# Kernel tuning notes

Measured on AMD Instinct MI355X. Metric: run time of the kernel, lower is better.

The kernel has to match this reference:

```python
import jax, jax.numpy as jnp
import numpy as np

B, IN, ED, PW, OUT, CL, NK = 2048, 4096, 8192, 2048, 256, 16, 32
MIX = 0.5

def _onehot_mask(key, n):
    # near-one-hot selector matrix [n, NK], as built by forward_update_masks
    idx = jax.random.choice(key, n, (NK,), replace=False)
    return jnp.zeros((n, NK), jnp.float32).at[idx, jnp.arange(NK)].set(1.0)

def setup_inputs():
    ks = jax.random.split(jax.random.key(0), 24)
    f = jnp.float32
    adj = (jax.random.uniform(ks[4], (IN, IN)) < 0.01).astype(f)
    adj = jnp.maximum(adj, adj.T).at[jnp.arange(IN), jnp.arange(IN)].set(1.0)
    return {
        'x_gene': jax.random.normal(ks[0], (B, IN), f),
        'x_invmea': jax.random.normal(ks[1], (B, IN), f),
        'x_curv': jax.random.normal(ks[2], (B, ED), f),
        'clinn': jax.random.normal(ks[3], (B, CL), f),
        'Adj': adj,
        'edge_mask': (jax.random.uniform(ks[5], (ED, IN)) < 0.005).astype(f),
        'pathway_mask': (jax.random.uniform(ks[6], (PW, ED)) < 0.02).astype(f),
        'top_gene_mask': _onehot_mask(ks[7], IN),
        'top_invmea_mask': _onehot_mask(ks[8], IN),
        'top_curv_mask': _onehot_mask(ks[9], ED),
        'top_path_mask': _onehot_mask(ks[10], PW),
        'W1': jnp.full((IN, IN), 0.05, f),
        'b1': 0.01 * jax.random.normal(ks[11], (IN,), f),
        'W2': jnp.full((ED, IN), 0.05, f),
        'b2': 0.01 * jax.random.normal(ks[12], (ED,), f),
        'W3': jnp.full((PW, ED), 0.05, f),
        'b3': 0.01 * jax.random.normal(ks[13], (PW,), f),
        'W4': 0.02 * jax.random.normal(ks[14], (OUT, PW), f),
        'b4': 0.01 * jax.random.normal(ks[15], (OUT,), f),
        'W5': 0.02 * jax.random.normal(ks[16], (OUT, OUT), f),
        'b5': 0.01 * jax.random.normal(ks[17], (OUT,), f),
        'W6': 0.05 * jax.random.normal(ks[18], (OUT, OUT + CL + 4 * NK), f),
        'W7': 0.05 * jax.random.normal(ks[19], (1, OUT), f),
        'mp11': MIX * jnp.ones(IN, f),
        'mp12': (1.0 - MIX) * jnp.ones(IN, f),
        'mp1': jnp.ones(IN, f),
        'mp21': MIX * jnp.ones(ED, f),
        'mp22': (1.0 - MIX) * jnp.ones(ED, f),
        'mp2': jnp.ones(ED, f),
        'mp3': jnp.ones(PW, f),
    }

def reference(x_gene, x_invmea, x_curv, clinn, Adj, edge_mask, pathway_mask,
              top_gene_mask, top_invmea_mask, top_curv_mask, top_path_mask,
              W1, b1, W2, b2, W3, b3, W4, b4, W5, b5, W6, W7,
              mp11, mp12, mp1, mp21, mp22, mp2, mp3):
    sg = jax.lax.stop_gradient
    sig = jax.nn.sigmoid
    kept_gene = sg(x_gene @ top_gene_mask)                     # [B,NK] gather-as-matmul
    x1 = sig(x_gene @ (W1 * Adj).T + b1)                       # masked linear [B,IN]
    x1 = x_invmea * (mp11 * mp1) + x1 * (mp12 * mp1)
    kept_invmea = sg(x1 @ top_invmea_mask)
    x1 = sig(x1 @ (W2 * edge_mask).T + b2)                     # [B,ED]
    x1 = x_curv * (mp21 * mp2) + x1 * (mp22 * mp2)
    kept_curv = sg(x1 @ top_curv_mask)
    x1 = sig(x1 @ (W3 * pathway_mask).T + b3)                  # [B,PW]
    x1 = x1 * mp3
    kept_path = sg(x1 @ top_path_mask)
    x1 = sig(x1 @ W4.T + b4)
    x1 = sig(x1 @ W5.T + b5)                                   # [B,OUT]
    x_cat = jnp.concatenate([x1, kept_gene, kept_invmea, kept_curv, kept_path, clinn], axis=1)
    lp = sig(x_cat @ W6.T)
    lp = lp - jnp.mean(lp, axis=1, keepdims=True)
    return lp @ W7.T                                           # [B,1]
```

## Files before the change

kernel.cpp:

```cpp
#include <hip/hip_runtime.h>

typedef unsigned short u16;
typedef __attribute__((ext_vector_type(4))) float f32x4;
typedef __attribute__((ext_vector_type(8))) short s16x8;

__device__ __forceinline__ u16 f2bf(float f) {
    union { float f; unsigned u; } c; c.f = f;
    return (u16)((c.u + 0x7fffu + ((c.u >> 16) & 1u)) >> 16);
}
__device__ __forceinline__ float bf2f(u16 u) {
    union { unsigned u; float f; } c; c.u = ((unsigned)u) << 16; return c.f;
}
__device__ __forceinline__ unsigned pk2(float a, float b) {
    return (unsigned)f2bf(a) | ((unsigned)f2bf(b) << 16);
}
__device__ __forceinline__ float sigm(float x) { return 1.0f / (1.0f + __expf(-x)); }
__device__ __forceinline__ void fma2(unsigned xv, float w, float& a0, float& a1) {
    union { float f; unsigned u; } lo, hi;
    lo.u = xv << 16; hi.u = xv & 0xFFFF0000u;
    a0 += w * lo.f; a1 += w * hi.f;
}

__device__ __forceinline__ void load16_g2l(const void* g, void* l) {
    __builtin_amdgcn_global_load_lds(
        (const __attribute__((address_space(1))) unsigned int*)(unsigned long long)g,
        (__attribute__((address_space(3))) unsigned int*)(unsigned int)(unsigned long long)l,
        16, 0, 0);
}

__global__ __launch_bounds__(256) void convF(const float* __restrict__ in,
                                             u16* __restrict__ out, unsigned n8) {
    unsigned i = blockIdx.x * 256u + threadIdx.x;
    if (i >= n8) return;
    float4 a = ((const float4*)in)[2 * i];
    float4 b = ((const float4*)in)[2 * i + 1];
    uint4 o;
    o.x = pk2(a.x, a.y); o.y = pk2(a.z, a.w);
    o.z = pk2(b.x, b.y); o.w = pk2(b.z, b.w);
    ((uint4*)out)[i] = o;
}

__global__ __launch_bounds__(256) void transpF(const float* __restrict__ in,
                                               u16* __restrict__ out, int Rr, int Cc) {
    __shared__ float t[64][65];
    const int r0 = blockIdx.y * 64, c0 = blockIdx.x * 64;
    const int tid = threadIdx.x;
#pragma unroll
    for (int i = 0; i < 16; i++) {
        int idx = tid + i * 256;
        int rr = idx >> 6, cc = idx & 63;
        t[rr][cc] = in[(size_t)(r0 + rr) * Cc + c0 + cc];
    }
    __syncthreads();
#pragma unroll
    for (int i = 0; i < 16; i++) {
        int idx = tid + i * 256;
        int cc = idx >> 6, rr = idx & 63;
        out[(size_t)(c0 + cc) * Rr + r0 + rr] = f2bf(t[rr][cc]);
    }
}

__global__ __launch_bounds__(256) void transpB(const u16* __restrict__ in,
                                               u16* __restrict__ out, int Rr, int Cc) {
    __shared__ u16 t[64][66];
    const int r0 = blockIdx.y * 64, c0 = blockIdx.x * 64;
    const int tid = threadIdx.x;
#pragma unroll
    for (int i = 0; i < 16; i++) {
        int idx = tid + i * 256;
        int rr = idx >> 6, cc = idx & 63;
        t[rr][cc] = in[(size_t)(r0 + rr) * Cc + c0 + cc];
    }
    __syncthreads();
#pragma unroll
    for (int i = 0; i < 16; i++) {
        int idx = tid + i * 256;
        int cc = idx >> 6, rr = idx & 63;
        out[(size_t)(c0 + cc) * Rr + r0 + rr] = t[rr][cc];
    }
}

__global__ __launch_bounds__(256) void ell_build(const float* __restrict__ M,
                                                 const float* __restrict__ W,
                                                 unsigned* __restrict__ ell,
                                                 int* __restrict__ cnt,
                                                 int C, int PAD, int R) {
    const int lane = threadIdx.x & 63;
    const int row = blockIdx.x * 4 + (threadIdx.x >> 6);
    if (row >= R) return;
    const float* mrow = M + (size_t)row * C;
    const float* wrow = W + (size_t)row * C;
    int n = 0;
    for (int c = lane * 4; c < C; c += 256) {
        float4 m = *(const float4*)(mrow + c);
        n += (m.x != 0.f) + (m.y != 0.f) + (m.z != 0.f) + (m.w != 0.f);
    }
    int pre = n;
#pragma unroll
    for (int off = 1; off < 64; off <<= 1) {
        int t = __shfl_up(pre, off, 64);
        if (lane >= off) pre += t;
    }
    int s = pre - n;
    unsigned* erow = ell + (size_t)row * PAD;
    for (int c = lane * 4; c < C; c += 256) {
        float4 m = *(const float4*)(mrow + c);
        if (m.x != 0.f) { if (s < PAD) erow[s] = ((unsigned)f2bf(wrow[c + 0]) << 16) | (unsigned)(c + 0); s++; }
        if (m.y != 0.f) { if (s < PAD) erow[s] = ((unsigned)f2bf(wrow[c + 1]) << 16) | (unsigned)(c + 1); s++; }
        if (m.z != 0.f) { if (s < PAD) erow[s] = ((unsigned)f2bf(wrow[c + 2]) << 16) | (unsigned)(c + 2); s++; }
        if (m.w != 0.f) { if (s < PAD) erow[s] = ((unsigned)f2bf(wrow[c + 3]) << 16) | (unsigned)(c + 3); s++; }
    }
    int tot = __shfl(pre, 63, 64);
    if (lane == 0) cnt[row] = tot > PAD ? PAD : tot;
}

template <int BPL>
__global__ __launch_bounds__(256) void spmm(const unsigned* __restrict__ ell,
                                            const int* __restrict__ cnt,
                                            const u16* __restrict__ xT,
                                            u16* __restrict__ outT,
                                            const float* __restrict__ bias,
                                            const float* __restrict__ c1a,
                                            const float* __restrict__ c1b,
                                            const float* __restrict__ c2a,
                                            const float* __restrict__ c2b,
                                            const u16* __restrict__ invT,
                                            int PAD) {
    const int lane = threadIdx.x & 63;
    const int wv = __builtin_amdgcn_readfirstlane((int)(threadIdx.x >> 6));
    const int j = blockIdx.y * 4 + wv;
    const int b0 = blockIdx.x * (64 * BPL) + lane * BPL;

    const unsigned* ep = ell + (size_t)j * PAD;
    int len = cnt[j];
    if (len > PAD) len = PAD;

    float acc[BPL];
#pragma unroll
    for (int i = 0; i < BPL; i++) acc[i] = 0.f;

    const int nfull = len >> 3;
    unsigned eA[8];
    if (nfull > 0) {
#pragma unroll
        for (int t = 0; t < 8; t++) eA[t] = ep[t];
    }
    for (int g = 0; g < nfull; g++) {
        unsigned eB[8];
        const bool more = (g + 1 < nfull);
        if (more) {
#pragma unroll
            for (int t = 0; t < 8; t++) eB[t] = ep[(g + 1) * 8 + t];
        }
        if (BPL == 8) {
            uint4 xv[8];
#pragma unroll
            for (int t = 0; t < 8; t++)
                xv[t] = *(const uint4*)(xT + ((size_t)(eA[t] & 0xFFFFu) << 11) + b0);
#pragma unroll
            for (int t = 0; t < 8; t++) {
                union { float f; unsigned u; } w; w.u = (eA[t] >> 16) << 16;
                fma2(xv[t].x, w.f, acc[0], acc[1]);
                fma2(xv[t].y, w.f, acc[2], acc[3]);
                fma2(xv[t].z, w.f, acc[4], acc[5]);
                fma2(xv[t].w, w.f, acc[6], acc[7]);
            }
        } else {
            uint2 xv[8];
#pragma unroll
            for (int t = 0; t < 8; t++)
                xv[t] = *(const uint2*)(xT + ((size_t)(eA[t] & 0xFFFFu) << 11) + b0);
#pragma unroll
            for (int t = 0; t < 8; t++) {
                union { float f; unsigned u; } w; w.u = (eA[t] >> 16) << 16;
                fma2(xv[t].x, w.f, acc[0], acc[1]);
                fma2(xv[t].y, w.f, acc[2], acc[3]);
            }
        }
        if (more) {
#pragma unroll
            for (int t = 0; t < 8; t++) eA[t] = eB[t];
        }
    }
    for (int s = nfull * 8; s < len; ++s) {
        unsigned e = ep[s];
        union { float f; unsigned u; } w; w.u = (e >> 16) << 16;
        const u16* xp = xT + ((size_t)(e & 0xFFFFu) << 11) + b0;
        if (BPL == 8) {
            uint4 xv = *(const uint4*)xp;
            fma2(xv.x, w.f, acc[0], acc[1]); fma2(xv.y, w.f, acc[2], acc[3]);
            fma2(xv.z, w.f, acc[4], acc[5]); fma2(xv.w, w.f, acc[6], acc[7]);
        } else {
            uint2 xv = *(const uint2*)xp;
            fma2(xv.x, w.f, acc[0], acc[1]); fma2(xv.y, w.f, acc[2], acc[3]);
        }
    }

    const float bi = bias[j];
    float c1 = 0.f;
    if (c1a) { c1 = c1a[j]; if (c1b) c1 *= c1b[j]; }
    float c2 = 1.f;
    if (c2a) { c2 = c2a[j]; if (c2b) c2 *= c2b[j]; }

    float v[BPL];
#pragma unroll
    for (int i = 0; i < BPL; i++) v[i] = sigm(acc[i] + bi) * c2;
    if (invT) {
        const unsigned long long* ip = (const unsigned long long*)(invT + ((size_t)j << 11) + b0);
#pragma unroll
        for (int h = 0; h < BPL / 4; h++) {
            unsigned long long iv = __builtin_nontemporal_load(ip + h);
            unsigned lo = (unsigned)iv, hi = (unsigned)(iv >> 32);
            union { float f; unsigned u; } g0, g1, g2, g3;
            g0.u = lo << 16; g1.u = lo & 0xFFFF0000u;
            g2.u = hi << 16; g3.u = hi & 0xFFFF0000u;
            v[4 * h + 0] += g0.f * c1; v[4 * h + 1] += g1.f * c1;
            v[4 * h + 2] += g2.f * c1; v[4 * h + 3] += g3.f * c1;
        }
    }
    unsigned long long* op = (unsigned long long*)(outT + ((size_t)j << 11) + b0);
#pragma unroll
    for (int h = 0; h < BPL / 4; h++) {
        unsigned long long ov = (unsigned long long)pk2(v[4 * h + 0], v[4 * h + 1])
                              | ((unsigned long long)pk2(v[4 * h + 2], v[4 * h + 3]) << 32);
        __builtin_nontemporal_store(ov, op + h);
    }
}

__global__ __launch_bounds__(256) void find_all(const float* __restrict__ m0, int n0,
                                                const float* __restrict__ m1, int n1,
                                                const float* __restrict__ m2, int n2,
                                                const float* __restrict__ m3, int n3,
                                                int* __restrict__ out) {
    __shared__ int red[256];
    const int g = blockIdx.x;
    const int which = g >> 5, k = g & 31;
    const float* mask; int n;
    if (which == 0)      { mask = m0; n = n0; }
    else if (which == 1) { mask = m1; n = n1; }
    else if (which == 2) { mask = m2; n = n2; }
    else                 { mask = m3; n = n3; }
    int best = -1;
    for (int i = threadIdx.x; i < n; i += 256)
        if (mask[(size_t)i * 32 + k] != 0.0f) best = i;
    red[threadIdx.x] = best;
    __syncthreads();
    for (int off = 128; off > 0; off >>= 1) {
        if (threadIdx.x < off) {
            int o = red[threadIdx.x + off];
            if (o > red[threadIdx.x]) red[threadIdx.x] = o;
        }
        __syncthreads();
    }
    if (threadIdx.x == 0) out[which * 32 + k] = red[0] < 0 ? 0 : red[0];
}

__global__ __launch_bounds__(256) void gatherFT(const float* __restrict__ src, int ld,
                                                const int* __restrict__ idx,
                                                u16* __restrict__ dstT) {
    int i = blockIdx.x * 256 + threadIdx.x;
    int kk = i >> 11, b = i & 2047;
    dstT[i] = f2bf(src[(size_t)b * ld + idx[kk]]);
}
__global__ __launch_bounds__(256) void gatherT(const u16* __restrict__ xT,
                                               const int* __restrict__ idx,
                                               u16* __restrict__ dstT) {
    int i = blockIdx.x * 256 + threadIdx.x;
    int kk = i >> 11, b = i & 2047;
    dstT[i] = xT[(size_t)idx[kk] * 2048 + b];
}

__global__ __launch_bounds__(256) void build_xcat(float* __restrict__ xcat,
                                                  const u16* __restrict__ x5,
                                                  const u16* __restrict__ kgT,
                                                  const u16* __restrict__ kiT,
                                                  const u16* __restrict__ kcT,
                                                  const u16* __restrict__ kpT,
                                                  const float* __restrict__ clinn) {
    int i = blockIdx.x * 256 + threadIdx.x;
    if (i >= 2048 * 400) return;
    int b = i / 400, c = i - b * 400;
    float v;
    if (c < 256)      v = bf2f(x5[b * 256 + c]);
    else if (c < 288) v = bf2f(kgT[(c - 256) * 2048 + b]);
    else if (c < 320) v = bf2f(kiT[(c - 288) * 2048 + b]);
    else if (c < 352) v = bf2f(kcT[(c - 320) * 2048 + b]);
    else if (c < 384) v = bf2f(kpT[(c - 352) * 2048 + b]);
    else              v = clinn[b * 16 + (c - 384)];
    xcat[i] = v;
}

template <int WR, int WC, int MF, int NF, int KC, int WPE>
__global__ __launch_bounds__(WR * WC * 64, WPE)
void gemm_t(const u16* __restrict__ A, const u16* __restrict__ W,
            u16* __restrict__ Out, const float* __restrict__ bias, int N, int K) {
    constexpr int NTHR = WR * WC * 64;
    constexpr int BM = WR * MF * 16;
    constexpr int BN = WC * NF * 16;
    constexpr int BK = KC * 32;
    constexpr int CPR = KC * 4;
    constexpr int MSK = CPR - 1;
    constexpr int CA = BM * CPR / NTHR;
    constexpr int CB = BN * CPR / NTHR;
    constexpr int L  = CA + CB;

    __shared__ u16 At[2][BM * BK];
    __shared__ u16 Bt[2][BN * BK];

    const int tid = threadIdx.x;
    const int lane = tid & 63;
    const int wave = tid >> 6;
    const int wr = wave / WC, wc = wave % WC;
    const int tn = blockIdx.x, tm = blockIdx.y;
    const int r16 = lane & 15;
    const int q = lane >> 4;

    const u16* aSrc[CA]; int aDst[CA];
#pragma unroll
    for (int j = 0; j < CA; j++) {
        int c = tid + j * NTHR;
        int r = c / CPR, p = c - r * CPR;
        aSrc[j] = A + (size_t)(tm * BM + r) * K + (p ^ (r & MSK)) * 8;
        aDst[j] = c * 8;
    }
    const u16* bSrc[CB]; int bDst[CB];
#pragma unroll
    for (int j = 0; j < CB; j++) {
        int c = tid + j * NTHR;
        int r = c / CPR, p = c - r * CPR;
        bSrc[j] = W + (size_t)(tn * BN + r) * K + (p ^ (r & MSK)) * 8;
        bDst[j] = c * 8;
    }
    int aRd[MF][KC], bRd[NF][KC];
#pragma unroll
    for (int mi = 0; mi < MF; mi++)
#pragma unroll
        for (int kc = 0; kc < KC; kc++)
            aRd[mi][kc] = (wr * MF * 16 + mi * 16 + r16) * BK + (((kc * 4 + q) ^ (r16 & MSK)) << 3);
#pragma unroll
    for (int ni = 0; ni < NF; ni++)
#pragma unroll
        for (int kc = 0; kc < KC; kc++)
            bRd[ni][kc] = (wc * NF * 16 + ni * 16 + r16) * BK + (((kc * 4 + q) ^ (r16 & MSK)) << 3);

    const int nIter = K / BK;

#define ISSUE(slot, it_)                                              \
    do {                                                              \
        const int k0_ = (it_) * BK;                                   \
        _Pragma("unroll")                                             \
        for (int j = 0; j < CA; j++)                                  \
            load16_g2l(aSrc[j] + k0_, &At[slot][aDst[j]]);            \
        _Pragma("unroll")                                             \
        for (int j = 0; j < CB; j++)                                  \
            load16_g2l(bSrc[j] + k0_, &Bt[slot][bDst[j]]);            \
    } while (0)

    ISSUE(0, 0);
    if (nIter > 1) ISSUE(1, 1);

    f32x4 acc[MF][NF];
#pragma unroll
    for (int i = 0; i < MF; i++)
#pragma unroll
        for (int j = 0; j < NF; j++) acc[i][j] = (f32x4){0.f, 0.f, 0.f, 0.f};

    for (int it = 0; it < nIter; ++it) {
        const int s = it & 1;
        if (it + 1 < nIter) __builtin_amdgcn_s_waitcnt(0xF70 | L);
        else                __builtin_amdgcn_s_waitcnt(0xF70);
        __asm__ volatile("" ::: "memory");
        __builtin_amdgcn_s_barrier();
        __asm__ volatile("" ::: "memory");

        s16x8 af[KC][MF], bfr[KC][NF];
#pragma unroll
        for (int kc = 0; kc < KC; kc++) {
#pragma unroll
            for (int mi = 0; mi < MF; mi++) af[kc][mi] = *(const s16x8*)(&At[s][aRd[mi][kc]]);
#pragma unroll
            for (int ni = 0; ni < NF; ni++) bfr[kc][ni] = *(const s16x8*)(&Bt[s][bRd[ni][kc]]);
        }
        __asm__ volatile("" ::: "memory");
        __builtin_amdgcn_s_waitcnt(0xC07F);
        __builtin_amdgcn_s_barrier();
        __asm__ volatile("" ::: "memory");

        if (it + 2 < nIter) ISSUE(s, it + 2);

#pragma unroll
        for (int kc = 0; kc < KC; kc++)
#pragma unroll
            for (int mi = 0; mi < MF; mi++)
#pragma unroll
                for (int ni = 0; ni < NF; ni++)
                    acc[mi][ni] = __builtin_amdgcn_mfma_f32_16x16x32_bf16(af[kc][mi], bfr[kc][ni], acc[mi][ni], 0, 0, 0);
    }
#undef ISSUE

#pragma unroll
    for (int ni = 0; ni < NF; ni++) {
        const int n = tn * BN + wc * NF * 16 + ni * 16 + r16;
        const float bi = bias ? bias[n] : 0.f;
#pragma unroll
        for (int mi = 0; mi < MF; mi++) {
#pragma unroll
            for (int rg = 0; rg < 4; rg++) {
                const int m = tm * BM + wr * MF * 16 + mi * 16 + q * 4 + rg;
                Out[(size_t)m * N + n] = f2bf(sigm(acc[mi][ni][rg] + bi));
            }
        }
    }
}

__global__ __launch_bounds__(256) void tail_k(const float* __restrict__ xcat,
                                              const float* __restrict__ W6,
                                              const float* __restrict__ W7,
                                              float* __restrict__ out) {
    __shared__ float xs[8 * 400];
    __shared__ float s1[4][8], s2[4][8], s3[4];
    const int tid = threadIdx.x;
    const int b0 = blockIdx.x * 8;
    for (int i = tid; i < 8 * 400; i += 256) {
        int r = i / 400, k = i - r * 400;
        xs[i] = xcat[(size_t)(b0 + r) * 400 + k];
    }
    __syncthreads();
    const int j = tid;
    float acc[8];
#pragma unroll
    for (int r = 0; r < 8; r++) acc[r] = 0.f;
    const float4* wrow = (const float4*)(W6 + (size_t)j * 400);
    for (int c = 0; c < 100; c++) {
        float4 wv = wrow[c];
        const float* wp = (const float*)&wv;
#pragma unroll
        for (int t = 0; t < 4; t++) {
            float w = wp[t];
            int k = c * 4 + t;
#pragma unroll
            for (int r = 0; r < 8; r++) acc[r] += w * xs[r * 400 + k];
        }
    }
    const float w7j = W7[j];
    const int lane = tid & 63, wave = tid >> 6;
    float t3 = w7j;
#pragma unroll
    for (int off = 32; off > 0; off >>= 1) t3 += __shfl_down(t3, off, 64);
    if (lane == 0) s3[wave] = t3;
#pragma unroll
    for (int r = 0; r < 8; r++) {
        float lp = sigm(acc[r]);
        float t1 = lp, t2 = lp * w7j;
#pragma unroll
        for (int off = 32; off > 0; off >>= 1) {
            t1 += __shfl_down(t1, off, 64);
            t2 += __shfl_down(t2, off, 64);
        }
        if (lane == 0) { s1[wave][r] = t1; s2[wave][r] = t2; }
    }
    __syncthreads();
    if (tid < 8) {
        float S1 = s1[0][tid] + s1[1][tid] + s1[2][tid] + s1[3][tid];
        float S2 = s2[0][tid] + s2[1][tid] + s2[2][tid] + s2[3][tid];
        float SW = s3[0] + s3[1] + s3[2] + s3[3];
        out[b0 + tid] = S2 - (S1 * (1.f / 256.f)) * SW;
    }
}

extern "C" void kernel_launch(void* const* d_in, const int* in_sizes, int n_in,
                              void* d_out, int out_size, void* d_ws, size_t ws_size,
                              hipStream_t stream) {
    const float* x_gene   = (const float*)d_in[0];
    const float* x_invmea = (const float*)d_in[1];
    const float* x_curv   = (const float*)d_in[2];
    const float* clinn    = (const float*)d_in[3];
    const float* Adj      = (const float*)d_in[4];
    const float* edge_m   = (const float*)d_in[5];
    const float* path_m   = (const float*)d_in[6];
    const float* tg_mask  = (const float*)d_in[7];
    const float* ti_mask  = (const float*)d_in[8];
    const float* tc_mask  = (const float*)d_in[9];
    const float* tp_mask  = (const float*)d_in[10];
    const float* W1 = (const float*)d_in[11];  const float* b1 = (const float*)d_in[12];
    const float* W2 = (const float*)d_in[13];  const float* b2 = (const float*)d_in[14];
    const float* W3 = (const float*)d_in[15];  const float* b3 = (const float*)d_in[16];
    const float* W4 = (const float*)d_in[17];  const float* b4 = (const float*)d_in[18];
    const float* W5 = (const float*)d_in[19];  const float* b5 = (const float*)d_in[20];
    const float* W6 = (const float*)d_in[21];
    const float* W7 = (const float*)d_in[22];
    const float* mp11 = (const float*)d_in[23];
    const float* mp12 = (const float*)d_in[24];
    const float* mp1  = (const float*)d_in[25];
    const float* mp21 = (const float*)d_in[26];
    const float* mp22 = (const float*)d_in[27];
    const float* mp2  = (const float*)d_in[28];
    const float* mp3  = (const float*)d_in[29];

    char* ws = (char*)d_ws;
    const float* nulf = nullptr;
    float* out = (float*)d_out;

    u16*  xTg   = (u16*)(ws + 0);
    float* xcat = (float*)(ws + 0);
    u16*  xinvT = (u16*)(ws + 16777216);
    u16*  xcvT  = (u16*)(ws + 33554432);
    u16*  x1T   = (u16*)(ws + 67108864);
    u16*  x2T   = (u16*)(ws + 83886080);
    u16*  x3T   = (u16*)(ws + 117440512);
    u16*  x3    = (u16*)(ws + 125829120);
    unsigned* ell1 = (unsigned*)(ws + 134217728);
    unsigned* ell2 = (unsigned*)(ws + 138412032);
    unsigned* ell3 = (unsigned*)(ws + 141557760);
    int* cnt1 = (int*)(ws + 144179200);
    int* cnt2 = (int*)(ws + 144195584);
    int* cnt3 = (int*)(ws + 144228352);
    int* idxg = (int*)(ws + 144236544);
    int* idxi = idxg + 32;
    int* idxc = idxg + 64;
    int* idxp = idxg + 96;
    u16* kgT  = (u16*)(ws + 144237056);
    u16* kiT  = (u16*)(ws + 144368128);
    u16* kcT  = (u16*)(ws + 144499200);
    u16* kpT  = (u16*)(ws + 144630272);
    u16* w4b  = (u16*)(ws + 144761344);
    u16* w5b  = (u16*)(ws + 145809920);
    u16* x4   = (u16*)(ws + 145940992);
    u16* x5   = (u16*)(ws + 146989568);

    find_all<<<128, 256, 0, stream>>>(tg_mask, 4096, ti_mask, 4096,
                                      tc_mask, 8192, tp_mask, 2048, idxg);
    gatherFT<<<256, 256, 0, stream>>>(x_gene, 4096, idxg, kgT);

    transpF<<<dim3(64, 32), 256, 0, stream>>>(x_gene, xTg, 2048, 4096);
    transpF<<<dim3(64, 32), 256, 0, stream>>>(x_invmea, xinvT, 2048, 4096);
    transpF<<<dim3(128, 32), 256, 0, stream>>>(x_curv, xcvT, 2048, 8192);

    ell_build<<<1024, 256, 0, stream>>>(Adj,    W1, ell1, cnt1, 4096, 256, 4096);
    ell_build<<<2048, 256, 0, stream>>>(edge_m, W2, ell2, cnt2, 4096,  96, 8192);
    ell_build<<<512,  256, 0, stream>>>(path_m, W3, ell3, cnt3, 8192, 320, 2048);

    convF<<<256, 256, 0, stream>>>(W4, w4b, 65536u);
    convF<<<32, 256, 0, stream>>>(W5, w5b, 8192u);

    spmm<8><<<dim3(4, 1024), 256, 0, stream>>>(ell1, cnt1, xTg, x1T, b1,
                                               mp11, mp1, mp12, mp1, xinvT, 256);
    gatherT<<<256, 256, 0, stream>>>(x1T, idxi, kiT);

    spmm<8><<<dim3(4, 2048), 256, 0, stream>>>(ell2, cnt2, x1T, x2T, b2,
                                               mp21, mp2, mp22, mp2, xcvT, 96);
    gatherT<<<256, 256, 0, stream>>>(x2T, idxc, kcT);

    spmm<4><<<dim3(8, 512), 256, 0, stream>>>(ell3, cnt3, x2T, x3T, b3,
                                              nulf, nulf, mp3, nulf, (const u16*)nullptr, 320);
    gatherT<<<256, 256, 0, stream>>>(x3T, idxp, kpT);
    transpB<<<dim3(32, 32), 256, 0, stream>>>(x3T, x3, 2048, 2048);

    gemm_t<2, 2, 2, 2, 2, 4><<<dim3(4, 32), 256, 0, stream>>>(x3, w4b, x4, b4, 256, 2048);
    gemm_t<2, 2, 2, 2, 2, 4><<<dim3(4, 32), 256, 0, stream>>>(x4, w5b, x5, b5, 256, 256);

    build_xcat<<<3200, 256, 0, stream>>>(xcat, x5, kgT, kiT, kcT, kpT, clinn);
    tail_k<<<256, 256, 0, stream>>>(xcat, W6, W7, out);
}
```

Measured before the change: 950.6 us.

## Merge preprocessing kernels into one launch, fold xcat build into tail, shrink spmm BPL

Folds the three input transposes, three ELL builds, the mask index search and the two weight conversions into a single prep_all kernel that dispatches on block ID. This removes many separate launches and the gaps between them. The xcat concatenation is now read directly inside tail_k, so the intermediate fp32 buffer and its extra kernel are gone. The first two spmm launches also drop from 8 to 4 batch elements per lane with twice the grid, trading per-thread reuse for more parallelism.

```diff
diff --git a/kernel.cpp b/kernel.cpp
--- a/kernel.cpp
+++ b/kernel.cpp
@@ -28,22 +28,9 @@
         16, 0, 0);
 }
 
-__global__ __launch_bounds__(256) void convF(const float* __restrict__ in,
-                                             u16* __restrict__ out, unsigned n8) {
-    unsigned i = blockIdx.x * 256u + threadIdx.x;
-    if (i >= n8) return;
-    float4 a = ((const float4*)in)[2 * i];
-    float4 b = ((const float4*)in)[2 * i + 1];
-    uint4 o;
-    o.x = pk2(a.x, a.y); o.y = pk2(a.z, a.w);
-    o.z = pk2(b.x, b.y); o.w = pk2(b.z, b.w);
-    ((uint4*)out)[i] = o;
-}
-
-__global__ __launch_bounds__(256) void transpF(const float* __restrict__ in,
-                                               u16* __restrict__ out, int Rr, int Cc) {
-    __shared__ float t[64][65];
-    const int r0 = blockIdx.y * 64, c0 = blockIdx.x * 64;
+__device__ void d_transpF(const float* __restrict__ in, u16* __restrict__ out,
+                          int Rr, int Cc, int bx, int by, float (*t)[65]) {
+    const int r0 = by * 64, c0 = bx * 64;
     const int tid = threadIdx.x;
 #pragma unroll
     for (int i = 0; i < 16; i++) {
@@ -60,33 +47,11 @@
     }
 }
 
-__global__ __launch_bounds__(256) void transpB(const u16* __restrict__ in,
-                                               u16* __restrict__ out, int Rr, int Cc) {
-    __shared__ u16 t[64][66];
-    const int r0 = blockIdx.y * 64, c0 = blockIdx.x * 64;
-    const int tid = threadIdx.x;
-#pragma unroll
-    for (int i = 0; i < 16; i++) {
-        int idx = tid + i * 256;
-        int rr = idx >> 6, cc = idx & 63;
-        t[rr][cc] = in[(size_t)(r0 + rr) * Cc + c0 + cc];
-    }
-    __syncthreads();
-#pragma unroll
-    for (int i = 0; i < 16; i++) {
-        int idx = tid + i * 256;
-        int cc = idx >> 6, rr = idx & 63;
-        out[(size_t)(c0 + cc) * Rr + r0 + rr] = t[rr][cc];
-    }
-}
-
-__global__ __launch_bounds__(256) void ell_build(const float* __restrict__ M,
-                                                 const float* __restrict__ W,
-                                                 unsigned* __restrict__ ell,
-                                                 int* __restrict__ cnt,
-                                                 int C, int PAD, int R) {
+__device__ void d_ell(const float* __restrict__ M, const float* __restrict__ W,
+                      unsigned* __restrict__ ell, int* __restrict__ cnt,
+                      int C, int PAD, int R, int bid) {
     const int lane = threadIdx.x & 63;
-    const int row = blockIdx.x * 4 + (threadIdx.x >> 6);
+    const int row = bid * 4 + (threadIdx.x >> 6);
     if (row >= R) return;
     const float* mrow = M + (size_t)row * C;
     const float* wrow = W + (size_t)row * C;
@@ -112,6 +77,80 @@
     }
     int tot = __shfl(pre, 63, 64);
     if (lane == 0) cnt[row] = tot > PAD ? PAD : tot;
+}
+
+__device__ void d_find(const float* __restrict__ mask, int n, int* __restrict__ outp,
+                       int* red) {
+    int best = -1;
+    for (int i = threadIdx.x; i < n; i += 256)
+        if (mask[(size_t)i * 32 + (blockIdx.x & 31)] != 0.0f) best = i;
+    red[threadIdx.x] = best;
+    __syncthreads();
+    for (int off = 128; off > 0; off >>= 1) {
+        if (threadIdx.x < off) {
+            int o = red[threadIdx.x + off];
+            if (o > red[threadIdx.x]) red[threadIdx.x] = o;
+        }
+        __syncthreads();
+    }
+    if (threadIdx.x == 0) *outp = red[0] < 0 ? 0 : red[0];
+}
+
+__device__ void d_conv(const float* __restrict__ in, u16* __restrict__ out,
+                       int bid, unsigned n8) {
+    unsigned i = bid * 256u + threadIdx.x;
+    if (i >= n8) return;
+    float4 a = ((const float4*)in)[2 * i];
+    float4 b = ((const float4*)in)[2 * i + 1];
+    uint4 o;
+    o.x = pk2(a.x, a.y); o.y = pk2(a.z, a.w);
+    o.z = pk2(b.x, b.y); o.w = pk2(b.z, b.w);
+    ((uint4*)out)[i] = o;
+}
+
+__global__ __launch_bounds__(256) void prep_all(
+    const float* __restrict__ xg_f, const float* __restrict__ xinv_f,
+    const float* __restrict__ xcv_f,
+    u16* __restrict__ xTg, u16* __restrict__ xinvT, u16* __restrict__ xcvT,
+    const float* __restrict__ Adj, const float* __restrict__ W1,
+    unsigned* __restrict__ ell1, int* __restrict__ cnt1,
+    const float* __restrict__ edge, const float* __restrict__ W2,
+    unsigned* __restrict__ ell2, int* __restrict__ cnt2,
+    const float* __restrict__ path, const float* __restrict__ W3,
+    unsigned* __restrict__ ell3, int* __restrict__ cnt3,
+    const float* __restrict__ m0, const float* __restrict__ m1,
+    const float* __restrict__ m2, const float* __restrict__ m3,
+    int* __restrict__ idx,
+    const float* __restrict__ W4, u16* __restrict__ w4b,
+    const float* __restrict__ W5, u16* __restrict__ w5b) {
+    __shared__ float tile[64][65];
+    int id = blockIdx.x;
+    if (id < 2048) { d_transpF(xg_f, xTg, 2048, 4096, id & 63, id >> 6, tile); return; }
+    id -= 2048;
+    if (id < 2048) { d_transpF(xinv_f, xinvT, 2048, 4096, id & 63, id >> 6, tile); return; }
+    id -= 2048;
+    if (id < 4096) { d_transpF(xcv_f, xcvT, 2048, 8192, id & 127, id >> 7, tile); return; }
+    id -= 4096;
+    if (id < 1024) { d_ell(Adj, W1, ell1, cnt1, 4096, 256, 4096, id); return; }
+    id -= 1024;
+    if (id < 2048) { d_ell(edge, W2, ell2, cnt2, 4096, 96, 8192, id); return; }
+    id -= 2048;
+    if (id < 512) { d_ell(path, W3, ell3, cnt3, 8192, 320, 2048, id); return; }
+    id -= 512;
+    if (id < 128) {
+        const float* mk; int n;
+        int which = id >> 5;
+        if (which == 0)      { mk = m0; n = 4096; }
+        else if (which == 1) { mk = m1; n = 4096; }
+        else if (which == 2) { mk = m2; n = 8192; }
+        else                 { mk = m3; n = 2048; }
+        d_find(mk, n, idx + which * 32 + (id & 31), (int*)tile);
+        return;
+    }
+    id -= 128;
+    if (id < 256) { d_conv(W4, w4b, id, 65536u); return; }
+    id -= 256;
+    d_conv(W5, w5b, id, 8192u);
 }
 
 template <int BPL>
@@ -227,34 +266,6 @@
     }
 }
 
-__global__ __launch_bounds__(256) void find_all(const float* __restrict__ m0, int n0,
-                                                const float* __restrict__ m1, int n1,
-                                                const float* __restrict__ m2, int n2,
-                                                const float* __restrict__ m3, int n3,
-                                                int* __restrict__ out) {
-    __shared__ int red[256];
-    const int g = blockIdx.x;
-    const int which = g >> 5, k = g & 31;
-    const float* mask; int n;
-    if (which == 0)      { mask = m0; n = n0; }
-    else if (which == 1) { mask = m1; n = n1; }
-    else if (which == 2) { mask = m2; n = n2; }
-    else                 { mask = m3; n = n3; }
-    int best = -1;
-    for (int i = threadIdx.x; i < n; i += 256)
-        if (mask[(size_t)i * 32 + k] != 0.0f) best = i;
-    red[threadIdx.x] = best;
-    __syncthreads();
-    for (int off = 128; off > 0; off >>= 1) {
-        if (threadIdx.x < off) {
-            int o = red[threadIdx.x + off];
-            if (o > red[threadIdx.x]) red[threadIdx.x] = o;
-        }
-        __syncthreads();
-    }
-    if (threadIdx.x == 0) out[which * 32 + k] = red[0] < 0 ? 0 : red[0];
-}
-
 __global__ __launch_bounds__(256) void gatherFT(const float* __restrict__ src, int ld,
                                                 const int* __restrict__ idx,
                                                 u16* __restrict__ dstT) {
@@ -270,24 +281,24 @@
     dstT[i] = xT[(size_t)idx[kk] * 2048 + b];
 }
 
-__global__ __launch_bounds__(256) void build_xcat(float* __restrict__ xcat,
-                                                  const u16* __restrict__ x5,
-                                                  const u16* __restrict__ kgT,
-                                                  const u16* __restrict__ kiT,
-                                                  const u16* __restrict__ kcT,
-                                                  const u16* __restrict__ kpT,
-                                                  const float* __restrict__ clinn) {
-    int i = blockIdx.x * 256 + threadIdx.x;
-    if (i >= 2048 * 400) return;
-    int b = i / 400, c = i - b * 400;
-    float v;
-    if (c < 256)      v = bf2f(x5[b * 256 + c]);
-    else if (c < 288) v = bf2f(kgT[(c - 256) * 2048 + b]);
-    else if (c < 320) v = bf2f(kiT[(c - 288) * 2048 + b]);
-    else if (c < 352) v = bf2f(kcT[(c - 320) * 2048 + b]);
-    else if (c < 384) v = bf2f(kpT[(c - 352) * 2048 + b]);
-    else              v = clinn[b * 16 + (c - 384)];
-    xcat[i] = v;
+__global__ __launch_bounds__(256) void transpB(const u16* __restrict__ in,
+                                               u16* __restrict__ out, int Rr, int Cc) {
+    __shared__ u16 t[64][66];
+    const int r0 = blockIdx.y * 64, c0 = blockIdx.x * 64;
+    const int tid = threadIdx.x;
+#pragma unroll
+    for (int i = 0; i < 16; i++) {
+        int idx = tid + i * 256;
+        int rr = idx >> 6, cc = idx & 63;
+        t[rr][cc] = in[(size_t)(r0 + rr) * Cc + c0 + cc];
+    }
+    __syncthreads();
+#pragma unroll
+    for (int i = 0; i < 16; i++) {
+        int idx = tid + i * 256;
+        int cc = idx >> 6, rr = idx & 63;
+        out[(size_t)(c0 + cc) * Rr + r0 + rr] = t[rr][cc];
+    }
 }
 
 template <int WR, int WC, int MF, int NF, int KC, int WPE>
@@ -413,7 +424,12 @@
     }
 }
 
-__global__ __launch_bounds__(256) void tail_k(const float* __restrict__ xcat,
+__global__ __launch_bounds__(256) void tail_k(const u16* __restrict__ x5,
+                                              const u16* __restrict__ kgT,
+                                              const u16* __restrict__ kiT,
+                                              const u16* __restrict__ kcT,
+                                              const u16* __restrict__ kpT,
+                                              const float* __restrict__ clinn,
                                               const float* __restrict__ W6,
                                               const float* __restrict__ W7,
                                               float* __restrict__ out) {
@@ -422,8 +438,16 @@
     const int tid = threadIdx.x;
     const int b0 = blockIdx.x * 8;
     for (int i = tid; i < 8 * 400; i += 256) {
-        int r = i / 400, k = i - r * 400;
-        xs[i] = xcat[(size_t)(b0 + r) * 400 + k];
+        int r = i / 400, c = i - r * 400;
+        int b = b0 + r;
+        float v;
+        if (c < 256)      v = bf2f(x5[b * 256 + c]);
+        else if (c < 288) v = bf2f(kgT[(c - 256) * 2048 + b]);
+        else if (c < 320) v = bf2f(kiT[(c - 288) * 2048 + b]);
+        else if (c < 352) v = bf2f(kcT[(c - 320) * 2048 + b]);
+        else if (c < 384) v = bf2f(kpT[(c - 352) * 2048 + b]);
+        else              v = clinn[b * 16 + (c - 384)];
+        xs[i] = v;
     }
     __syncthreads();
     const int j = tid;
@@ -502,7 +526,6 @@
     float* out = (float*)d_out;
 
     u16*  xTg   = (u16*)(ws + 0);
-    float* xcat = (float*)(ws + 0);
     u16*  xinvT = (u16*)(ws + 16777216);
     u16*  xcvT  = (u16*)(ws + 33554432);
     u16*  x1T   = (u16*)(ws + 67108864);
@@ -528,26 +551,17 @@
     u16* x4   = (u16*)(ws + 145940992);
     u16* x5   = (u16*)(ws + 146989568);
 
-    find_all<<<128, 256, 0, stream>>>(tg_mask, 4096, ti_mask, 4096,
-                                      tc_mask, 8192, tp_mask, 2048, idxg);
+    prep_all<<<12192, 256, 0, stream>>>(
+        x_gene, x_invmea, x_curv, xTg, xinvT, xcvT,
+        Adj, W1, ell1, cnt1, edge_m, W2, ell2, cnt2, path_m, W3, ell3, cnt3,
+        tg_mask, ti_mask, tc_mask, tp_mask, idxg, W4, w4b, W5, w5b);
     gatherFT<<<256, 256, 0, stream>>>(x_gene, 4096, idxg, kgT);
 
-    transpF<<<dim3(64, 32), 256, 0, stream>>>(x_gene, xTg, 2048, 4096);
-    transpF<<<dim3(64, 32), 256, 0, stream>>>(x_invmea, xinvT, 2048, 4096);
-    transpF<<<dim3(128, 32), 256, 0, stream>>>(x_curv, xcvT, 2048, 8192);
-
-    ell_build<<<1024, 256, 0, stream>>>(Adj,    W1, ell1, cnt1, 4096, 256, 4096);
-    ell_build<<<2048, 256, 0, stream>>>(edge_m, W2, ell2, cnt2, 4096,  96, 8192);
-    ell_build<<<512,  256, 0, stream>>>(path_m, W3, ell3, cnt3, 8192, 320, 2048);
-
-    convF<<<256, 256, 0, stream>>>(W4, w4b, 65536u);
-    convF<<<32, 256, 0, stream>>>(W5, w5b, 8192u);
-
-    spmm<8><<<dim3(4, 1024), 256, 0, stream>>>(ell1, cnt1, xTg, x1T, b1,
+    spmm<4><<<dim3(8, 1024), 256, 0, stream>>>(ell1, cnt1, xTg, x1T, b1,
                                                mp11, mp1, mp12, mp1, xinvT, 256);
     gatherT<<<256, 256, 0, stream>>>(x1T, idxi, kiT);
 
-    spmm<8><<<dim3(4, 2048), 256, 0, stream>>>(ell2, cnt2, x1T, x2T, b2,
+    spmm<4><<<dim3(8, 2048), 256, 0, stream>>>(ell2, cnt2, x1T, x2T, b2,
                                                mp21, mp2, mp22, mp2, xcvT, 96);
     gatherT<<<256, 256, 0, stream>>>(x2T, idxc, kcT);
 
@@ -559,6 +573,5 @@
     gemm_t<2, 2, 2, 2, 2, 4><<<dim3(4, 32), 256, 0, stream>>>(x3, w4b, x4, b4, 256, 2048);
     gemm_t<2, 2, 2, 2, 2, 4><<<dim3(4, 32), 256, 0, stream>>>(x4, w5b, x5, b5, 256, 256);
 
-    build_xcat<<<3200, 256, 0, stream>>>(xcat, x5, kgT, kiT, kcT, kpT, clinn);
-    tail_k<<<256, 256, 0, stream>>>(xcat, W6, W7, out);
-}
+    tail_k<<<256, 256, 0, stream>>>(x5, kgT, kiT, kcT, kpT, clinn, W6, W7, out);
+}
```

New measurement: 940.8 us. Within noise of the previous version (-1.0%).
